# Optimization experiments

Hardware: AMD Instinct MI355X
Metric: run time of the kernel (lower is better)

Reference implementation:

```python
import jax, jax.numpy as jnp
import numpy as np

B, T, D, H, C, M = 128, 96, 256, 256, 8, 64
COMB = 4 * D + H  # z, z_prime, x_i, global_dynamics, h


def setup_inputs() -> dict:
    key = jax.random.key(0)
    ks = jax.random.split(key, 24)
    X = jax.random.normal(ks[0], (B, T, D), jnp.float32)
    X_last = jax.random.normal(ks[1], (B, T, D), jnp.float32)
    Mask = jax.random.bernoulli(ks[2], 0.5, (B, T, D)).astype(jnp.float32)
    Delta = jax.random.uniform(ks[3], (B, T, D), jnp.float32, 0.0, 5.0)
    X_last_b = jax.random.normal(ks[4], (B, T, D), jnp.float32)
    Delta_b = jax.random.uniform(ks[5], (B, T, D), jnp.float32, 0.0, 5.0)
    x = jnp.stack([X, X_last, Mask, Delta, X_last_b, Delta_b], axis=1)  # [B,6,T,D]
    X_mean = jax.random.normal(ks[6], (1, T, D), jnp.float32)
    clusters = jax.random.randint(ks[7], (D,), 1, C + 1, jnp.int64)
    s = 1.0 / np.sqrt(COMB)
    def U(k, shape, sc):
        return jax.random.uniform(k, shape, jnp.float32, -sc, sc)
    params = {
        'W_i': U(ks[8], (H, COMB), s), 'b_i': U(ks[9], (H,), s),
        'W_f': U(ks[10], (H, COMB), s), 'b_f': U(ks[11], (H,), s),
        'W_o': U(ks[12], (H, COMB), s), 'b_o': U(ks[13], (H,), s),
        'W_c': U(ks[14], (H, COMB), s), 'b_c': U(ks[15], (H,), s),
        'W_fc': U(ks[16], (D, H), 1.0 / np.sqrt(H)), 'b_fc': U(ks[17], (D,), 1.0 / np.sqrt(H)),
        'gz_w': U(ks[18], (D,), 1.0 / np.sqrt(D)), 'gz_b': U(ks[19], (D,), 1.0 / np.sqrt(D)),
        'gzp_w': U(ks[20], (D,), 1.0 / np.sqrt(D)), 'gzp_b': U(ks[21], (D,), 1.0 / np.sqrt(D)),
        'memory': jax.random.uniform(ks[22], (C, M, D), jnp.float32, -1.0 / np.sqrt(M), 1.0 / np.sqrt(M)),
    }
    k2 = jax.random.split(ks[23], 2)
    params['local_w'] = jax.random.uniform(k2[0], (3, D), jnp.float32, -1.0 / np.sqrt(3.0), 1.0 / np.sqrt(3.0))
    params['global_w'] = jax.random.uniform(k2[1], (C,), jnp.float32, -1.0 / np.sqrt(C), 1.0 / np.sqrt(C))
    return dict(x=x, X_mean=X_mean, clusters=clusters, **params)


def reference(x, X_mean, clusters, W_i, b_i, W_f, b_f, W_o, b_o, W_c, b_c,
              W_fc, b_fc, gz_w, gz_b, gzp_w, gzp_b, memory, local_w, global_w):
    # cluster one-hot feature masks: [C, D] (cluster ids are 1-based)
    cmask = (clusters[None, :] == jnp.arange(1, C + 1, dtype=clusters.dtype)[:, None]).astype(x.dtype)

    X, X_last, Mask, Delta, X_last_b, Delta_b = [x[:, i] for i in range(6)]  # each [B,T,D]
    xm = X_mean[0]  # [T,D]

    def step(carry, inp):
        h, c = carry
        xt, xl, xlb, m, d, db, mean = inp
        # FilterLinear with eye filter == diagonal linear; GRU-D decay
        dz = jnp.exp(-jax.nn.relu(d * gz_w + gz_b))
        dzp = jnp.exp(-jax.nn.relu(db * gzp_w + gzp_b))
        z = m * xt + (1 - m) * (dz * xl + (1 - dz) * mean)
        zp = m * xt + (1 - m) * (dzp * xlb + (1 - dzp) * mean)
        x_i = h @ W_fc.T + b_fc  # [B,D]
        local_stats = local_w[0] * z + local_w[1] * zp + local_w[2] * x_i  # [B,D]
        # per-cluster masked local stats -> memory attention
        li = local_stats[:, None, :] * cmask[None]              # [B,C,D]
        scores = jnp.einsum('cmd,bcd->bcm', memory, li)          # [B,C,M]
        s = jax.nn.softmax(scores, axis=-1)
        gd = jnp.einsum('bcm,cmd->bcd', s, memory)               # [B,C,D]
        gd = jnp.einsum('bcd,c->bd', gd, global_w)               # [B,D]
        combined = jnp.concatenate([z, zp, x_i, gd, h], axis=1)  # [B,4D+H]
        i = jax.nn.sigmoid(combined @ W_i.T + b_i)
        f = jax.nn.sigmoid(combined @ W_f.T + b_f)
        o = jax.nn.sigmoid(combined @ W_o.T + b_o)
        ct = jnp.tanh(combined @ W_c.T + b_c)
        c = f * c + i * ct
        h = o * jnp.tanh(c)
        out = h @ W_fc.T + b_fc
        return (h, c), out

    h0 = jnp.zeros((x.shape[0], H), x.dtype)
    c0 = jnp.zeros((x.shape[0], H), x.dtype)
    xs = (X.transpose(1, 0, 2), X_last.transpose(1, 0, 2), X_last_b.transpose(1, 0, 2),
          Mask.transpose(1, 0, 2), Delta.transpose(1, 0, 2), Delta_b.transpose(1, 0, 2), xm)
    _, outs = jax.lax.scan(step, (h0, c0), xs)
    return outs.transpose(1, 0, 2)  # [B,T,D]
```

## Files before the change

### kernel.cpp

```cpp
#include <hip/hip_runtime.h>
#include <hip/hip_bf16.h>
#include <hip/hip_fp16.h>
#include <cstdint>
#include <cstddef>


#define PLANE 24576

using bf16_t = __hip_bfloat16;
typedef __bf16 bf16x8 __attribute__((ext_vector_type(8)));
typedef float  f32x4  __attribute__((ext_vector_type(4)));
typedef unsigned int u32x4 __attribute__((ext_vector_type(4)));

__device__ __forceinline__ float  b2f(bf16_t v){ return __bfloat162float(v); }
__device__ __forceinline__ bf16_t f2b(float v){ return __float2bfloat16(v); }
__device__ __forceinline__ float ldF(const void* p, size_t i, int f32){
  return f32 ? ((const float*)p)[i] : b2f(((const bf16_t*)p)[i]);
}
__device__ __forceinline__ bf16x8 ld_frag(const void* p){
  union { uint4 u; bf16x8 v; } c;
  c.u = *(const uint4*)p;
  return c.v;
}
__device__ __forceinline__ bf16x8 u2b(u32x4 u){
  union { u32x4 u; bf16x8 v; } c; c.u = u; return c.v;
}
__device__ __forceinline__ f32x4 mfma_bf16(bf16x8 a, bf16x8 b, f32x4 c){
  return __builtin_amdgcn_mfma_f32_16x16x32_bf16(a, b, c, 0, 0, 0);
}

__device__ __forceinline__ u32x4 ld_cg(const void* p){
  u32x4 r;
  asm volatile("global_load_dwordx4 %0, %1, off sc0 sc1"
               : "=v"(r) : "v"(p) : "memory");
  return r;
}
__device__ __forceinline__ void st_cg(void* p, u32x4 v){
  asm volatile("global_store_dwordx4 %0, %1, off sc0 sc1"
               :: "v"(p), "v"(v) : "memory");
}
__device__ __forceinline__ int ld_cg_u16(const void* p){
  int r;
  asm volatile("global_load_ushort %0, %1, off sc0 sc1"
               : "=v"(r) : "v"(p) : "memory");
  return r;
}
__device__ __forceinline__ void st_flag(int* p, int v){
  asm volatile("global_store_dword %0, %1, off sc0 sc1"
               :: "v"(p), "v"(v) : "memory");
}
__device__ __forceinline__ int ld_flag(const int* p){
  int r;
  asm volatile("global_load_dword %0, %1, off sc0 sc1\n\ts_waitcnt vmcnt(0)"
               : "=v"(r) : "v"(p) : "memory");
  return r;
}
__device__ __forceinline__ void vm_wait0(){
  asm volatile("s_waitcnt vmcnt(0)" ::: "memory");
  __builtin_amdgcn_sched_barrier(0);
}
__device__ __forceinline__ float h2f_bits(int u){
  union{ unsigned short s; __half h; } c; c.s = (unsigned short)u;
  return __half2float(c.h);
}

__global__ __launch_bounds__(64) void k_detect(
    const uint32_t* __restrict__ xu, const uint32_t* __restrict__ clu,
    int* __restrict__ flags)
{
  __shared__ int cnt[2];
  int t = threadIdx.x;
  if (t < 2) cnt[t] = 0;
  __syncthreads();
  uint32_t v = xu[2*PLANE + t];
  if (v == 0u || v == 0x3F800000u) atomicAdd(&cnt[0], 1);
  if (clu[2*t + 1] == 0u) atomicAdd(&cnt[1], 1);
  __syncthreads();
  if (t == 0){
    flags[0] = (cnt[0] >= 48) ? 1 : 0;
    flags[1] = (cnt[1] >= 60) ? 1 : 0;
  }
}

__global__ __launch_bounds__(256) void k_zero(int* __restrict__ bar){
  bar[blockIdx.x*256 + threadIdx.x] = 0;
}

__global__ __launch_bounds__(256) void k_canon(
    const void* __restrict__ Wfc, const void* __restrict__ Xmean,
    const void* __restrict__ bfc, const void* __restrict__ localw,
    const void* __restrict__ globalw, const void* __restrict__ gzw,
    const void* __restrict__ gzb, const void* __restrict__ gzpw,
    const void* __restrict__ gzpb, const int* __restrict__ flags,
    bf16_t* __restrict__ WfcC, bf16_t* __restrict__ XmC,
    bf16_t* __restrict__ bfcC, bf16_t* __restrict__ lwC,
    bf16_t* __restrict__ gwC, float* __restrict__ gzC)
{
  const int f32 = flags[0];
  int i = blockIdx.x*256 + threadIdx.x;
  if (i < 65536) WfcC[i] = f2b(ldF(Wfc, i, f32));
  if (i < 24576) XmC[i]  = f2b(ldF(Xmean, i, f32));
  if (i < 256)   bfcC[i] = f2b(ldF(bfc, i, f32));
  if (i < 768)   lwC[i]  = f2b(ldF(localw, i, f32));
  if (i < 8)     gwC[i]  = f2b(ldF(globalw, i, f32));
  if (i < 256){
    gzC[i]       = ldF(gzw,  i, f32);
    gzC[256 + i] = ldF(gzb,  i, f32);
    gzC[512 + i] = ldF(gzpw, i, f32);
    gzC[768 + i] = ldF(gzpb, i, f32);
  }
}

__global__ __launch_bounds__(256) void k_fold(
    const void* __restrict__ Wi, const void* __restrict__ Wf,
    const void* __restrict__ Wo, const void* __restrict__ Wc,
    const void* __restrict__ bi, const void* __restrict__ bfg,
    const void* __restrict__ bo, const void* __restrict__ bcg,
    const void* __restrict__ Wfc, const void* __restrict__ bfc,
    const int* __restrict__ flags,
    bf16_t* __restrict__ U, bf16_t* __restrict__ Uz, float* __restrict__ bias2)
{
  const int f32 = flags[0];
  int n = blockIdx.x; int g = n & 3; int j = n >> 2;
  const void* Wg = (g==0)?Wi:(g==1)?Wf:(g==2)?Wo:Wc;
  const void* bg = (g==0)?bi:(g==1)?bfg:(g==2)?bo:bcg;
  const size_t wb = (size_t)j*1280;
  int k = threadIdx.x;
  float acc = 0.f;
  for (int d=0; d<256; ++d)
    acc += ldF(Wg, wb+512+d, f32) * ldF(Wfc, (size_t)d*256+k, f32);
  U[(size_t)n*512 + k]        = f2b(acc + ldF(Wg, wb+1024+k, f32));
  U[(size_t)n*512 + 256 + k]  = f2b(ldF(Wg, wb+768+k, f32));
  Uz[(size_t)n*512 + k]       = f2b(ldF(Wg, wb+k, f32));
  Uz[(size_t)n*512 + 256 + k] = f2b(ldF(Wg, wb+256+k, f32));
  __shared__ float red[256];
  red[k] = ldF(Wg, wb+512+k, f32) * ldF(bfc, k, f32);
  __syncthreads();
  for (int s=128; s>0; s>>=1){ if (k<s) red[k]+=red[k+s]; __syncthreads(); }
  if (k==0) bias2[n] = red[0] + ldF(bg, j, f32);
}

__global__ __launch_bounds__(256) void k_foldG(
    const void* __restrict__ Wi, const void* __restrict__ Wf,
    const void* __restrict__ Wo, const void* __restrict__ Wc,
    const void* __restrict__ memory, const int* __restrict__ flags,
    bf16_t* __restrict__ G)
{
  const int f32 = flags[0];
  __shared__ float wrow[4][256];
  int j = blockIdx.x; int tid = threadIdx.x;
  const void* Wg[4] = {Wi,Wf,Wo,Wc};
  for (int g=0; g<4; ++g)
    wrow[g][tid] = ldF(Wg[g], (size_t)j*1280 + 768 + tid, f32);
  __syncthreads();
  for (int half=0; half<2; ++half){
    int cm = half*256 + tid;
    float a0=0,a1=0,a2=0,a3=0;
    for (int d=0; d<256; ++d){
      float mv = ldF(memory, (size_t)cm*256 + d, f32);
      a0 += wrow[0][d]*mv; a1 += wrow[1][d]*mv;
      a2 += wrow[2][d]*mv; a3 += wrow[3][d]*mv;
    }
    G[(size_t)(4*j+0)*512 + cm] = f2b(a0);
    G[(size_t)(4*j+1)*512 + cm] = f2b(a1);
    G[(size_t)(4*j+2)*512 + cm] = f2b(a2);
    G[(size_t)(4*j+3)*512 + cm] = f2b(a3);
  }
}

__global__ __launch_bounds__(256) void k_foldQ(
    const int* __restrict__ clusters, const void* __restrict__ memory,
    const bf16_t* __restrict__ lwC, const bf16_t* __restrict__ WfcC,
    const bf16_t* __restrict__ bfcC, const int* __restrict__ flags,
    bf16_t* __restrict__ Mem2, bf16_t* __restrict__ Qbf, float* __restrict__ qb)
{
  const int f32 = flags[0], i64 = flags[1];
  const int cm = blockIdx.x; const int c = cm >> 6;
  const int tid = threadIdx.x;
  __shared__ float ml2[256];
  __shared__ float red[256];
  int cv = i64 ? clusters[2*tid] : clusters[tid];
  float mv = (cv == c+1) ? ldF(memory, (size_t)cm*256 + tid, f32) : 0.f;
  Mem2[(size_t)cm*256 + tid] = f2b(mv);
  float m2 = mv * b2f(lwC[512 + tid]);
  ml2[tid] = m2;
  red[tid] = m2 * b2f(bfcC[tid]);
  __syncthreads();
  float acc = 0.f;
  for (int d=0; d<256; ++d)
    acc += ml2[d] * b2f(WfcC[(size_t)d*256 + tid]);
  Qbf[(size_t)cm*256 + tid] = f2b(acc);
  for (int s=128; s>0; s>>=1){ if (tid<s) red[tid]+=red[tid+s]; __syncthreads(); }
  if (tid==0) qb[cm] = red[0];
}

__global__ __launch_bounds__(256) void k_zzp(
    const void* __restrict__ x, const bf16_t* __restrict__ XmC,
    const float* __restrict__ gzC, const bf16_t* __restrict__ lwC,
    const int* __restrict__ flags,
    bf16_t* __restrict__ Zcat, bf16_t* __restrict__ Zl)
{
  const int f32 = flags[0];
  int r = blockIdx.x;
  int t = r >> 7, b = r & 127, d = threadIdx.x;
  size_t base = (size_t)b*6*PLANE + (size_t)t*256 + d;
  float xt = ldF(x, base          , f32);
  float xl = ldF(x, base +   PLANE, f32);
  float mk = ldF(x, base + 2*PLANE, f32);
  float de = ldF(x, base + 3*PLANE, f32);
  float xlb= ldF(x, base + 4*PLANE, f32);
  float deb= ldF(x, base + 5*PLANE, f32);
  float mean = b2f(XmC[t*256+d]);
  float dz  = expf(-fmaxf(0.f, de *gzC[d]     + gzC[256+d]));
  float dzp = expf(-fmaxf(0.f, deb*gzC[512+d] + gzC[768+d]));
  float z  = mk*xt + (1.f-mk)*(dz *xl  + (1.f-dz )*mean);
  float zp = mk*xt + (1.f-mk)*(dzp*xlb + (1.f-dzp)*mean);
  Zcat[(size_t)r*512 + d]       = f2b(z);
  Zcat[(size_t)r*512 + 256 + d] = f2b(zp);
  Zl[(size_t)r*256 + d] = f2b(b2f(lwC[d])*z + b2f(lwC[256+d])*zp);
}

__global__ __launch_bounds__(256) void k_mega(
    const bf16_t* __restrict__ gwC,
    const bf16_t* __restrict__ U, const bf16_t* __restrict__ G,
    const bf16_t* __restrict__ Qbf, const bf16_t* __restrict__ Uz,
    const float* __restrict__ bias2, const bf16_t* __restrict__ Mem2,
    const float* __restrict__ qb, const bf16_t* __restrict__ Zcat,
    const bf16_t* __restrict__ Zl, const bf16_t* __restrict__ WfcC,
    const bf16_t* __restrict__ bfcC, const int* __restrict__ flags,
    __half* __restrict__ zc, __half* __restrict__ SzM,
    bf16_t* __restrict__ hSeq, bf16_t* __restrict__ tSeq,
    int* __restrict__ bar, void* __restrict__ outv)
{
  __shared__ bf16_t Us[64][264];
  __shared__ bf16_t Gs[64][520];
  __shared__ bf16_t Qs[64][264];
  __shared__ bf16_t hS[16][264];
  __shared__ bf16_t tS[16][520];
  __shared__ bf16_t tO[16][64];
  __shared__ bf16_t hO[16][16];

  const int bid = blockIdx.x;
  const int tid = threadIdx.x;
  const int W = tid>>6, l = tid&63, q = l>>4, cl = l&15;
  int* zcflag  = bar + 512;
  int* szmflag = bar + 576;

  if (bid < 128){
    const int g = bid & 7, s = bid >> 3;
    const int r0 = g*16;
    const int n0 = s*64;
    int* barA = bar + g*64;
    int* barB = bar + g*64 + 32;

    for (int i=tid; i<64*32; i+=256){ int r=i>>5, c8=(i&31)*8;
      *(uint4*)(&Us[r][c8]) = *(const uint4*)(U + (size_t)(n0+r)*512 + c8); }
    for (int i=tid; i<64*64; i+=256){ int r=i>>6, c8=(i&63)*8;
      *(uint4*)(&Gs[r][c8]) = *(const uint4*)(G + (size_t)(n0+r)*512 + c8); }
    if (s<8)
      for (int i=tid; i<64*32; i+=256){ int r=i>>5, c8=(i&31)*8;
        *(uint4*)(&Qs[r][c8]) = *(const uint4*)(Qbf + (size_t)(s*64+r)*256 + c8); }
    const float gw_c = (s<8)? b2f(gwC[s]) : 0.f;
    const bool sc_wave = (s<8) && (W==0);
    float creg[4] = {0.f,0.f,0.f,0.f};
    __syncthreads();

    for (int t=0; t<96; ++t){
      if (W==0){
        const int* fp = nullptr; int need = 0; bool act = false;
        if (l < 16){ fp = barA + l; need = t; act = (t>0); }
        else if (l < 20){ fp = zcflag + 4*s + (l-16); need = t+1; act = true; }
        else if (l < 24){ fp = szmflag + 4*s + (l-20); need = t+1; act = (s<8); }
        int f;
        do { f = act ? ld_flag(fp) : 0x7fffffff; } while (__any(f < need));
        if (t>0){
          const bf16_t* hsrc = hSeq + (size_t)t*128*256 + (size_t)r0*256;
          u32x4 hv[8];
#pragma unroll
          for (int k=0;k<8;++k){ int c=l+64*k;
            hv[k] = ld_cg(hsrc + (size_t)(c>>5)*256 + (c&31)*8); }
          vm_wait0();
#pragma unroll
          for (int k=0;k<8;++k){ int c=l+64*k;
            *(u32x4*)(&hS[c>>5][(c&31)*8]) = hv[k]; }
        } else {
#pragma unroll
          for (int k=0;k<8;++k){ int c=l+64*k;
            *(u32x4*)(&hS[c>>5][(c&31)*8]) = (u32x4){0,0,0,0}; }
        }
      }
      __syncthreads();
      int zr[4];
#pragma unroll
      for (int rr=0; rr<4; ++rr)
        zr[rr] = ld_cg_u16(zc + ((size_t)(t*128)+r0+q*4+rr)*1024 + n0 + W*16 + cl);
      if (sc_wave){
        int sr[16];
#pragma unroll
        for (int nt=0; nt<4; ++nt)
#pragma unroll
          for (int rr=0; rr<4; ++rr)
            sr[nt*4+rr] = ld_cg_u16(
              SzM + ((size_t)(t*128)+r0+q*4+rr)*512 + s*64 + nt*16 + cl);
        f32x4 sa[4];
#pragma unroll
        for (int nt=0;nt<4;++nt) sa[nt]=(f32x4){0.f,0.f,0.f,0.f};
#pragma unroll
        for (int ks=0; ks<8; ++ks){
          bf16x8 a = ld_frag(&hS[cl][ks*32 + q*8]);
#pragma unroll
          for (int nt=0; nt<4; ++nt)
            sa[nt] = mfma_bf16(a, ld_frag(&Qs[nt*16+cl][ks*32 + q*8]), sa[nt]);
        }
        vm_wait0();
#pragma unroll
        for (int nt=0; nt<4; ++nt)
#pragma unroll
          for (int rr=0; rr<4; ++rr) sa[nt][rr] += h2f_bits(sr[nt*4+rr]);
#pragma unroll
        for (int rr=0; rr<4; ++rr){
          float mx = fmaxf(fmaxf(sa[0][rr],sa[1][rr]), fmaxf(sa[2][rr],sa[3][rr]));
          mx = fmaxf(mx, __shfl_xor(mx,1));
          mx = fmaxf(mx, __shfl_xor(mx,2));
          mx = fmaxf(mx, __shfl_xor(mx,4));
          mx = fmaxf(mx, __shfl_xor(mx,8));
          float e0=expf(sa[0][rr]-mx), e1=expf(sa[1][rr]-mx);
          float e2=expf(sa[2][rr]-mx), e3=expf(sa[3][rr]-mx);
          float sm = e0+e1+e2+e3;
          sm += __shfl_xor(sm,1); sm += __shfl_xor(sm,2);
          sm += __shfl_xor(sm,4); sm += __shfl_xor(sm,8);
          float sc = gw_c/sm;
          tO[q*4+rr][ 0+cl] = f2b(e0*sc);
          tO[q*4+rr][16+cl] = f2b(e1*sc);
          tO[q*4+rr][32+cl] = f2b(e2*sc);
          tO[q*4+rr][48+cl] = f2b(e3*sc);
        }
        bf16_t* tdst = tSeq + (size_t)t*128*512 + (size_t)r0*512 + s*64;
#pragma unroll
        for (int k=0;k<2;++k){ int c=l+64*k;
          u32x4 v = *(u32x4*)(&tO[c>>3][(c&7)*8]);
          st_cg(tdst + (size_t)(c>>3)*512 + (c&7)*8, v); }
        vm_wait0();
        if (l==0) st_flag(barB + s, t+1);
      }
      f32x4 acc = {0.f,0.f,0.f,0.f};
#pragma unroll
      for (int ks=0; ks<8; ++ks)
        acc = mfma_bf16(ld_frag(&hS[cl][ks*32 + q*8]),
                        ld_frag(&Us[W*16+cl][ks*32 + q*8]), acc);
      if (W==1){
        const int* fp = barB + (l&7);
        int v;
        do { int f = ld_flag(fp); v = (l<8)? f : 0x7fffffff; } while (__any(v < t+1));
        const bf16_t* tsrc = tSeq + (size_t)t*128*512 + (size_t)r0*512;
        u32x4 tv[16];
#pragma unroll
        for (int k=0;k<16;++k){ int c=l+64*k;
          tv[k] = ld_cg(tsrc + (size_t)(c>>6)*512 + (c&63)*8); }
        vm_wait0();
#pragma unroll
        for (int k=0;k<16;++k){ int c=l+64*k;
          *(u32x4*)(&tS[c>>6][(c&63)*8]) = tv[k]; }
      }
      __syncthreads();
#pragma unroll
      for (int ks=0; ks<16; ++ks)
        acc = mfma_bf16(ld_frag(&tS[cl][ks*32 + q*8]),
                        ld_frag(&Gs[W*16+cl][ks*32 + q*8]), acc);
      vm_wait0();
#pragma unroll
      for (int rr=0; rr<4; ++rr) acc[rr] += h2f_bits(zr[rr]);
      const int base = l & ~3;
#pragma unroll
      for (int rr=0; rr<4; ++rr){
        float p = acc[rr];
        float pi = __shfl(p, base+0);
        float pf = __shfl(p, base+1);
        float po = __shfl(p, base+2);
        float pc = __shfl(p, base+3);
        float iv = 1.f/(1.f+expf(-pi));
        float fv = 1.f/(1.f+expf(-pf));
        float ov = 1.f/(1.f+expf(-po));
        float cv = tanhf(pc);
        float cn = fv*creg[rr] + iv*cv;
        creg[rr] = cn;
        float hv = ov * tanhf(cn);
        if ((l&3)==0)
          hO[q*4+rr][W*4 + (cl>>2)] = f2b(hv);
      }
      __syncthreads();
      if (W==0){
        if (l < 32){
          u32x4 v = *(u32x4*)(&hO[l>>1][(l&1)*8]);
          st_cg(hSeq + (size_t)(t+1)*128*256 + (size_t)(r0+(l>>1))*256
                     + s*16 + (l&1)*8, v);
        }
        vm_wait0();
        if (l==0) st_flag(barA + s, t+1);
      }
    }
  } else if (bid < 192){
    const int a = bid - 128;
    const int n0a = a*16;
    bf16_t (*BS)[520] = (bf16_t(*)[520])&Gs[0][0];
    __half (*zT)[16]  = (__half(*)[16])&Qs[0][0];
    for (int i=tid; i<16*64; i+=256){ int r=i>>6, c8=(i&63)*8;
      *(uint4*)(&BS[r][c8]) = *(const uint4*)(Uz + (size_t)(n0a+r)*512 + c8); }
    const float bias = bias2[n0a + cl];
    __syncthreads();
    for (int t=0; t<96; ++t){
      f32x4 a0={0.f,0.f,0.f,0.f}, a1={0.f,0.f,0.f,0.f};
      const bf16_t* ar0 = Zcat + ((size_t)t*128 + W*32 + cl)*512;
      const bf16_t* ar1 = ar0 + (size_t)16*512;
#pragma unroll
      for (int ks=0; ks<16; ++ks){
        bf16x8 b = ld_frag(&BS[cl][ks*32 + q*8]);
        a0 = mfma_bf16(ld_frag(ar0 + ks*32 + q*8), b, a0);
        a1 = mfma_bf16(ld_frag(ar1 + ks*32 + q*8), b, a1);
      }
#pragma unroll
      for (int rr=0; rr<4; ++rr){
        zT[W*32      + q*4 + rr][cl] = __float2half(a0[rr] + bias);
        zT[W*32 + 16 + q*4 + rr][cl] = __float2half(a1[rr] + bias);
      }
      __syncthreads();
      { int row = tid>>1, half = tid&1;
        u32x4 v = *(u32x4*)(&zT[row][half*8]);
        st_cg(zc + ((size_t)t*128+row)*1024 + n0a + half*8, v);
      }
      vm_wait0();
      __syncthreads();
      if (tid==0) st_flag(zcflag + a, t+1);
    }
  } else if (bid < 224){
    const int a2 = bid - 192;
    const int cm0 = a2*16;
    bf16_t (*BS)[520] = (bf16_t(*)[520])&Gs[0][0];
    __half (*zT)[16]  = (__half(*)[16])&Qs[0][0];
    for (int i=tid; i<16*32; i+=256){ int r=i>>5, c8=(i&31)*8;
      *(uint4*)(&BS[r][c8]) = *(const uint4*)(Mem2 + (size_t)(cm0+r)*256 + c8); }
    const float bias = qb[cm0 + cl];
    __syncthreads();
    for (int t=0; t<96; ++t){
      f32x4 a0={0.f,0.f,0.f,0.f}, a1={0.f,0.f,0.f,0.f};
      const bf16_t* ar0 = Zl + ((size_t)t*128 + W*32 + cl)*256;
      const bf16_t* ar1 = ar0 + (size_t)16*256;
#pragma unroll
      for (int ks=0; ks<8; ++ks){
        bf16x8 b = ld_frag(&BS[cl][ks*32 + q*8]);
        a0 = mfma_bf16(ld_frag(ar0 + ks*32 + q*8), b, a0);
        a1 = mfma_bf16(ld_frag(ar1 + ks*32 + q*8), b, a1);
      }
#pragma unroll
      for (int rr=0; rr<4; ++rr){
        zT[W*32      + q*4 + rr][cl] = __float2half(a0[rr] + bias);
        zT[W*32 + 16 + q*4 + rr][cl] = __float2half(a1[rr] + bias);
      }
      __syncthreads();
      { int row = tid>>1, half = tid&1;
        u32x4 v = *(u32x4*)(&zT[row][half*8]);
        st_cg(SzM + ((size_t)t*128+row)*512 + cm0 + half*8, v);
      }
      vm_wait0();
      __syncthreads();
      if (tid==0) st_flag(szmflag + a2, t+1);
    }
  } else {
    const int a3 = bid - 224;
    const int oc0 = a3*16;
    bf16_t (*BS)[520] = (bf16_t(*)[520])&Gs[0][0];
    for (int i=tid; i<16*32; i+=256){ int r=i>>5, c8=(i&31)*8;
      *(uint4*)(&BS[r][c8]) = *(const uint4*)(WfcC + (size_t)(oc0+r)*256 + c8); }
    const float bias = b2f(bfcC[oc0 + cl]);
    const int f32o = flags[0];
    __syncthreads();
    for (int t=0; t<96; ++t){
      const int* f1 = bar + (l>>4)*64 + (l&15);
      const int* f2 = bar + ((l>>4)+4)*64 + (l&15);
      int fa, fb;
      do { fa = ld_flag(f1); fb = ld_flag(f2); }
      while (__any((fa < t+1) || (fb < t+1)));
      u32x4 av0[8], av1[8];
      const bf16_t* hr0 = hSeq + ((size_t)(t+1)*128 + W*32 + cl)*256;
      const bf16_t* hr1 = hr0 + (size_t)16*256;
#pragma unroll
      for (int ks=0; ks<8; ++ks){
        av0[ks] = ld_cg(hr0 + ks*32 + q*8);
        av1[ks] = ld_cg(hr1 + ks*32 + q*8);
      }
      vm_wait0();
      f32x4 o0={0.f,0.f,0.f,0.f}, o1={0.f,0.f,0.f,0.f};
#pragma unroll
      for (int ks=0; ks<8; ++ks){
        bf16x8 b = ld_frag(&BS[cl][ks*32 + q*8]);
        o0 = mfma_bf16(u2b(av0[ks]), b, o0);
        o1 = mfma_bf16(u2b(av1[ks]), b, o1);
      }
#pragma unroll
      for (int rr=0; rr<4; ++rr){
        int b0 = W*32 + q*4 + rr;
        int b1 = b0 + 16;
        float v0 = o0[rr] + bias;
        float v1 = o1[rr] + bias;
        size_t ob0 = ((size_t)b0*96 + t)*256 + oc0 + cl;
        size_t ob1 = ((size_t)b1*96 + t)*256 + oc0 + cl;
        if (f32o){ ((float*)outv)[ob0] = v0; ((float*)outv)[ob1] = v1; }
        else     { ((bf16_t*)outv)[ob0] = f2b(v0); ((bf16_t*)outv)[ob1] = f2b(v1); }
      }
    }
  }
}

extern "C" void kernel_launch(void* const* d_in, const int* in_sizes, int n_in,
                              void* d_out, int out_size, void* d_ws, size_t ws_size,
                              hipStream_t stream)
{
  const void* x       = d_in[0];
  const void* Xmean   = d_in[1];
  const int*  clusters= (const int*)d_in[2];
  const void* Wi  = d_in[3];
  const void* bi  = d_in[4];
  const void* Wf  = d_in[5];
  const void* bfp = d_in[6];
  const void* Wo  = d_in[7];
  const void* bo  = d_in[8];
  const void* Wc  = d_in[9];
  const void* bcp = d_in[10];
  const void* Wfc = d_in[11];
  const void* bfc = d_in[12];
  const void* gzw = d_in[13];
  const void* gzb = d_in[14];
  const void* gzpw= d_in[15];
  const void* gzpb= d_in[16];
  const void* memory = d_in[17];
  const void* localw = d_in[18];
  const void* globalw= d_in[19];
  (void)in_sizes; (void)n_in; (void)out_size; (void)ws_size;

  char* ws = (char*)d_ws;
  size_t off = 0;
  auto take = [&](size_t bytes)->char*{
    char* p = ws + off; off = (off + bytes + 255) & ~(size_t)255; return p; };
  int*    flags  = (int*)   take(16);
  int*    bar    = (int*)   take(1024*4);
  bf16_t* U      = (bf16_t*)take((size_t)1024*512*2);
  bf16_t* Uz     = (bf16_t*)take((size_t)1024*512*2);
  bf16_t* G      = (bf16_t*)take((size_t)1024*512*2);
  bf16_t* WfcC   = (bf16_t*)take((size_t)65536*2);
  bf16_t* XmC    = (bf16_t*)take((size_t)24576*2);
  bf16_t* bfcC   = (bf16_t*)take(256*2);
  bf16_t* lwC    = (bf16_t*)take(768*2);
  bf16_t* gwC    = (bf16_t*)take(8*2);
  float*  gzC    = (float*) take(1024*4);
  float*  bias2  = (float*) take(1024*4);
  bf16_t* Mem2   = (bf16_t*)take((size_t)512*256*2);
  bf16_t* Qbf    = (bf16_t*)take((size_t)512*256*2);
  float*  qb     = (float*) take(512*4);
  __half* zc     = (__half*)take((size_t)12288*1024*2);
  __half* SzM    = (__half*)take((size_t)12288*512*2);
  bf16_t* Zcat   = (bf16_t*)take((size_t)12288*512*2);
  bf16_t* Zl     = (bf16_t*)take((size_t)12288*256*2);
  bf16_t* tSeq   = (bf16_t*)take((size_t)96*128*512*2);
  bf16_t* hSeq   = (bf16_t*)take((size_t)97*128*256*2);

  k_detect<<<1,    64, 0,stream>>>((const uint32_t*)x, (const uint32_t*)clusters, flags);
  k_zero  <<<4,    256,0,stream>>>(bar);
  k_canon <<<256,  256,0,stream>>>(Wfc, Xmean, bfc, localw, globalw,
                                   gzw, gzb, gzpw, gzpb, flags,
                                   WfcC, XmC, bfcC, lwC, gwC, gzC);
  k_fold  <<<1024, 256,0,stream>>>(Wi,Wf,Wo,Wc, bi,bfp,bo,bcp, Wfc,bfc, flags,
                                   U, Uz, bias2);
  k_foldG <<<256,  256,0,stream>>>(Wi,Wf,Wo,Wc, memory, flags, G);
  k_foldQ <<<512,  256,0,stream>>>(clusters, memory, lwC, WfcC, bfcC, flags,
                                   Mem2, Qbf, qb);
  k_zzp   <<<12288,256,0,stream>>>(x, XmC, gzC, lwC, flags, Zcat, Zl);
  k_mega  <<<240,  256,0,stream>>>(gwC, U, G, Qbf, Uz, bias2, Mem2, qb,
                                   Zcat, Zl, WfcC, bfcC, flags,
                                   zc, SzM, hSeq, tSeq, bar, d_out);
}
```

Before: 1.093 ms.

## Merge prep kernels, widen producer tiles, and stage score and output through LDS

Folds the zero, fold, foldG, foldQ and zzp launches into k_canon plus one block-indexed k_prep kernel, cutting launch count. In k_mega the zc, SzM and output producer blocks now each compute 64- or 32-column tiles, which drops the grid from 240 to 160 blocks and reduces the number of flags to poll. Outputs are staged in LDS so they can be written as coalesced 16-byte stores. The SzM scores are prefetched into shared memory by a spare wave, and the gate nonlinearities are applied once per lane before the shuffle. The fewer, larger producer blocks each carry more serial work per timestep, which could lengthen the recurrent critical path.

After: 1.498 ms. +37.1%, slower.

```diff
diff --git a/kernel.cpp b/kernel.cpp
--- a/kernel.cpp
+++ b/kernel.cpp
@@ -28,6 +28,14 @@
 __device__ __forceinline__ f32x4 mfma_bf16(bf16x8 a, bf16x8 b, f32x4 c){
   return __builtin_amdgcn_mfma_f32_16x16x32_bf16(a, b, c, 0, 0, 0);
 }
+__device__ __forceinline__ unsigned pkb(float a, float b){
+  union{ bf16_t h; unsigned short u;} ca, cb; ca.h=f2b(a); cb.h=f2b(b);
+  return (unsigned)ca.u | ((unsigned)cb.u<<16);
+}
+__device__ __forceinline__ float h2f_bits(int u){
+  union{ unsigned short s; __half h; } c; c.s = (unsigned short)u;
+  return __half2float(c.h);
+}
 
 __device__ __forceinline__ u32x4 ld_cg(const void* p){
   u32x4 r;
@@ -58,10 +66,6 @@
 __device__ __forceinline__ void vm_wait0(){
   asm volatile("s_waitcnt vmcnt(0)" ::: "memory");
   __builtin_amdgcn_sched_barrier(0);
-}
-__device__ __forceinline__ float h2f_bits(int u){
-  union{ unsigned short s; __half h; } c; c.s = (unsigned short)u;
-  return __half2float(c.h);
 }
 
 __global__ __launch_bounds__(64) void k_detect(
@@ -82,10 +86,6 @@
   }
 }
 
-__global__ __launch_bounds__(256) void k_zero(int* __restrict__ bar){
-  bar[blockIdx.x*256 + threadIdx.x] = 0;
-}
-
 __global__ __launch_bounds__(256) void k_canon(
     const void* __restrict__ Wfc, const void* __restrict__ Xmean,
     const void* __restrict__ bfc, const void* __restrict__ localw,
@@ -94,10 +94,12 @@
     const void* __restrict__ gzpb, const int* __restrict__ flags,
     bf16_t* __restrict__ WfcC, bf16_t* __restrict__ XmC,
     bf16_t* __restrict__ bfcC, bf16_t* __restrict__ lwC,
-    bf16_t* __restrict__ gwC, float* __restrict__ gzC)
+    bf16_t* __restrict__ gwC, float* __restrict__ gzC,
+    int* __restrict__ bar)
 {
   const int f32 = flags[0];
   int i = blockIdx.x*256 + threadIdx.x;
+  if (blockIdx.x < 4) bar[i] = 0;
   if (i < 65536) WfcC[i] = f2b(ldF(Wfc, i, f32));
   if (i < 24576) XmC[i]  = f2b(ldF(Xmean, i, f32));
   if (i < 256)   bfcC[i] = f2b(ldF(bfc, i, f32));
@@ -111,113 +113,98 @@
   }
 }
 
-__global__ __launch_bounds__(256) void k_fold(
+__global__ __launch_bounds__(256) void k_prep(
     const void* __restrict__ Wi, const void* __restrict__ Wf,
     const void* __restrict__ Wo, const void* __restrict__ Wc,
     const void* __restrict__ bi, const void* __restrict__ bfg,
     const void* __restrict__ bo, const void* __restrict__ bcg,
     const void* __restrict__ Wfc, const void* __restrict__ bfc,
-    const int* __restrict__ flags,
-    bf16_t* __restrict__ U, bf16_t* __restrict__ Uz, float* __restrict__ bias2)
-{
-  const int f32 = flags[0];
-  int n = blockIdx.x; int g = n & 3; int j = n >> 2;
-  const void* Wg = (g==0)?Wi:(g==1)?Wf:(g==2)?Wo:Wc;
-  const void* bg = (g==0)?bi:(g==1)?bfg:(g==2)?bo:bcg;
-  const size_t wb = (size_t)j*1280;
-  int k = threadIdx.x;
-  float acc = 0.f;
-  for (int d=0; d<256; ++d)
-    acc += ldF(Wg, wb+512+d, f32) * ldF(Wfc, (size_t)d*256+k, f32);
-  U[(size_t)n*512 + k]        = f2b(acc + ldF(Wg, wb+1024+k, f32));
-  U[(size_t)n*512 + 256 + k]  = f2b(ldF(Wg, wb+768+k, f32));
-  Uz[(size_t)n*512 + k]       = f2b(ldF(Wg, wb+k, f32));
-  Uz[(size_t)n*512 + 256 + k] = f2b(ldF(Wg, wb+256+k, f32));
-  __shared__ float red[256];
-  red[k] = ldF(Wg, wb+512+k, f32) * ldF(bfc, k, f32);
-  __syncthreads();
-  for (int s=128; s>0; s>>=1){ if (k<s) red[k]+=red[k+s]; __syncthreads(); }
-  if (k==0) bias2[n] = red[0] + ldF(bg, j, f32);
-}
-
-__global__ __launch_bounds__(256) void k_foldG(
-    const void* __restrict__ Wi, const void* __restrict__ Wf,
-    const void* __restrict__ Wo, const void* __restrict__ Wc,
-    const void* __restrict__ memory, const int* __restrict__ flags,
-    bf16_t* __restrict__ G)
-{
-  const int f32 = flags[0];
-  __shared__ float wrow[4][256];
-  int j = blockIdx.x; int tid = threadIdx.x;
-  const void* Wg[4] = {Wi,Wf,Wo,Wc};
-  for (int g=0; g<4; ++g)
-    wrow[g][tid] = ldF(Wg[g], (size_t)j*1280 + 768 + tid, f32);
-  __syncthreads();
-  for (int half=0; half<2; ++half){
-    int cm = half*256 + tid;
-    float a0=0,a1=0,a2=0,a3=0;
-    for (int d=0; d<256; ++d){
-      float mv = ldF(memory, (size_t)cm*256 + d, f32);
-      a0 += wrow[0][d]*mv; a1 += wrow[1][d]*mv;
-      a2 += wrow[2][d]*mv; a3 += wrow[3][d]*mv;
-    }
-    G[(size_t)(4*j+0)*512 + cm] = f2b(a0);
-    G[(size_t)(4*j+1)*512 + cm] = f2b(a1);
-    G[(size_t)(4*j+2)*512 + cm] = f2b(a2);
-    G[(size_t)(4*j+3)*512 + cm] = f2b(a3);
-  }
-}
-
-__global__ __launch_bounds__(256) void k_foldQ(
-    const int* __restrict__ clusters, const void* __restrict__ memory,
+    const void* __restrict__ memory, const int* __restrict__ clusters,
+    const void* __restrict__ x,
+    const bf16_t* __restrict__ XmC, const float* __restrict__ gzC,
     const bf16_t* __restrict__ lwC, const bf16_t* __restrict__ WfcC,
     const bf16_t* __restrict__ bfcC, const int* __restrict__ flags,
-    bf16_t* __restrict__ Mem2, bf16_t* __restrict__ Qbf, float* __restrict__ qb)
-{
-  const int f32 = flags[0], i64 = flags[1];
-  const int cm = blockIdx.x; const int c = cm >> 6;
-  const int tid = threadIdx.x;
-  __shared__ float ml2[256];
-  __shared__ float red[256];
-  int cv = i64 ? clusters[2*tid] : clusters[tid];
-  float mv = (cv == c+1) ? ldF(memory, (size_t)cm*256 + tid, f32) : 0.f;
-  Mem2[(size_t)cm*256 + tid] = f2b(mv);
-  float m2 = mv * b2f(lwC[512 + tid]);
-  ml2[tid] = m2;
-  red[tid] = m2 * b2f(bfcC[tid]);
-  __syncthreads();
-  float acc = 0.f;
-  for (int d=0; d<256; ++d)
-    acc += ml2[d] * b2f(WfcC[(size_t)d*256 + tid]);
-  Qbf[(size_t)cm*256 + tid] = f2b(acc);
-  for (int s=128; s>0; s>>=1){ if (tid<s) red[tid]+=red[tid+s]; __syncthreads(); }
-  if (tid==0) qb[cm] = red[0];
-}
-
-__global__ __launch_bounds__(256) void k_zzp(
-    const void* __restrict__ x, const bf16_t* __restrict__ XmC,
-    const float* __restrict__ gzC, const bf16_t* __restrict__ lwC,
-    const int* __restrict__ flags,
+    bf16_t* __restrict__ U, bf16_t* __restrict__ Uz,
+    float* __restrict__ bias2, bf16_t* __restrict__ G,
+    bf16_t* __restrict__ Mem2, bf16_t* __restrict__ Qbf,
+    float* __restrict__ qb,
     bf16_t* __restrict__ Zcat, bf16_t* __restrict__ Zl)
 {
-  const int f32 = flags[0];
-  int r = blockIdx.x;
-  int t = r >> 7, b = r & 127, d = threadIdx.x;
-  size_t base = (size_t)b*6*PLANE + (size_t)t*256 + d;
-  float xt = ldF(x, base          , f32);
-  float xl = ldF(x, base +   PLANE, f32);
-  float mk = ldF(x, base + 2*PLANE, f32);
-  float de = ldF(x, base + 3*PLANE, f32);
-  float xlb= ldF(x, base + 4*PLANE, f32);
-  float deb= ldF(x, base + 5*PLANE, f32);
-  float mean = b2f(XmC[t*256+d]);
-  float dz  = expf(-fmaxf(0.f, de *gzC[d]     + gzC[256+d]));
-  float dzp = expf(-fmaxf(0.f, deb*gzC[512+d] + gzC[768+d]));
-  float z  = mk*xt + (1.f-mk)*(dz *xl  + (1.f-dz )*mean);
-  float zp = mk*xt + (1.f-mk)*(dzp*xlb + (1.f-dzp)*mean);
-  Zcat[(size_t)r*512 + d]       = f2b(z);
-  Zcat[(size_t)r*512 + 256 + d] = f2b(zp);
-  Zl[(size_t)r*256 + d] = f2b(b2f(lwC[d])*z + b2f(lwC[256+d])*zp);
+  __shared__ float sA[4][256];
+  __shared__ float red[256];
+  const int f32 = flags[0], i64 = flags[1];
+  const int bid = blockIdx.x, tid = threadIdx.x;
+
+  if (bid < 1024){
+    int n = bid; int g = n & 3; int j = n >> 2;
+    const void* Wg = (g==0)?Wi:(g==1)?Wf:(g==2)?Wo:Wc;
+    const void* bg = (g==0)?bi:(g==1)?bfg:(g==2)?bo:bcg;
+    const size_t wb = (size_t)j*1280;
+    int k = tid;
+    float acc = 0.f;
+    for (int d=0; d<256; ++d)
+      acc += ldF(Wg, wb+512+d, f32) * ldF(Wfc, (size_t)d*256+k, f32);
+    U[(size_t)n*512 + k]        = f2b(acc + ldF(Wg, wb+1024+k, f32));
+    U[(size_t)n*512 + 256 + k]  = f2b(ldF(Wg, wb+768+k, f32));
+    Uz[(size_t)n*512 + k]       = f2b(ldF(Wg, wb+k, f32));
+    Uz[(size_t)n*512 + 256 + k] = f2b(ldF(Wg, wb+256+k, f32));
+    red[k] = ldF(Wg, wb+512+k, f32) * ldF(bfc, k, f32);
+    __syncthreads();
+    for (int s=128; s>0; s>>=1){ if (k<s) red[k]+=red[k+s]; __syncthreads(); }
+    if (k==0) bias2[n] = red[0] + ldF(bg, j, f32);
+  } else if (bid < 1280){
+    int j = bid - 1024;
+    const void* Wg[4] = {Wi,Wf,Wo,Wc};
+    for (int g=0; g<4; ++g)
+      sA[g][tid] = ldF(Wg[g], (size_t)j*1280 + 768 + tid, f32);
+    __syncthreads();
+    for (int half=0; half<2; ++half){
+      int cm = half*256 + tid;
+      float a0=0,a1=0,a2=0,a3=0;
+      for (int d=0; d<256; ++d){
+        float mv = ldF(memory, (size_t)cm*256 + d, f32);
+        a0 += sA[0][d]*mv; a1 += sA[1][d]*mv;
+        a2 += sA[2][d]*mv; a3 += sA[3][d]*mv;
+      }
+      G[(size_t)(4*j+0)*512 + cm] = f2b(a0);
+      G[(size_t)(4*j+1)*512 + cm] = f2b(a1);
+      G[(size_t)(4*j+2)*512 + cm] = f2b(a2);
+      G[(size_t)(4*j+3)*512 + cm] = f2b(a3);
+    }
+  } else if (bid < 1792){
+    const int cm = bid - 1280; const int c = cm >> 6;
+    int cv = i64 ? clusters[2*tid] : clusters[tid];
+    float mv = (cv == c+1) ? ldF(memory, (size_t)cm*256 + tid, f32) : 0.f;
+    Mem2[(size_t)cm*256 + tid] = f2b(mv);
+    float m2 = mv * b2f(lwC[512 + tid]);
+    sA[0][tid] = m2;
+    red[tid] = m2 * b2f(bfcC[tid]);
+    __syncthreads();
+    float acc = 0.f;
+    for (int d=0; d<256; ++d)
+      acc += sA[0][d] * b2f(WfcC[(size_t)d*256 + tid]);
+    Qbf[(size_t)cm*256 + tid] = f2b(acc);
+    for (int s=128; s>0; s>>=1){ if (tid<s) red[tid]+=red[tid+s]; __syncthreads(); }
+    if (tid==0) qb[cm] = red[0];
+  } else {
+    int r = bid - 1792;
+    int t = r >> 7, b = r & 127, d = tid;
+    size_t base = (size_t)b*6*PLANE + (size_t)t*256 + d;
+    float xt = ldF(x, base          , f32);
+    float xl = ldF(x, base +   PLANE, f32);
+    float mk = ldF(x, base + 2*PLANE, f32);
+    float de = ldF(x, base + 3*PLANE, f32);
+    float xlb= ldF(x, base + 4*PLANE, f32);
+    float deb= ldF(x, base + 5*PLANE, f32);
+    float mean = b2f(XmC[t*256+d]);
+    float dz  = expf(-fmaxf(0.f, de *gzC[d]     + gzC[256+d]));
+    float dzp = expf(-fmaxf(0.f, deb*gzC[512+d] + gzC[768+d]));
+    float z  = mk*xt + (1.f-mk)*(dz *xl  + (1.f-dz )*mean);
+    float zp = mk*xt + (1.f-mk)*(dzp*xlb + (1.f-dzp)*mean);
+    Zcat[(size_t)r*512 + d]       = f2b(z);
+    Zcat[(size_t)r*512 + 256 + d] = f2b(zp);
+    Zl[(size_t)r*256 + d] = f2b(b2f(lwC[d])*z + b2f(lwC[256+d])*zp);
+  }
 }
 
 __global__ __launch_bounds__(256) void k_mega(
@@ -232,19 +219,20 @@
     bf16_t* __restrict__ hSeq, bf16_t* __restrict__ tSeq,
     int* __restrict__ bar, void* __restrict__ outv)
 {
-  __shared__ bf16_t Us[64][264];
-  __shared__ bf16_t Gs[64][520];
-  __shared__ bf16_t Qs[64][264];
-  __shared__ bf16_t hS[16][264];
-  __shared__ bf16_t tS[16][520];
+  __shared__ bf16_t Us[64][260];
+  __shared__ bf16_t Gs[64][516];
+  __shared__ bf16_t Qs[64][260];
+  __shared__ bf16_t hS[16][260];
+  __shared__ bf16_t tS[16][516];
   __shared__ bf16_t tO[16][64];
   __shared__ bf16_t hO[16][16];
+  __shared__ __half smS[16][68];
 
   const int bid = blockIdx.x;
   const int tid = threadIdx.x;
   const int W = tid>>6, l = tid&63, q = l>>4, cl = l&15;
   int* zcflag  = bar + 512;
-  int* szmflag = bar + 576;
+  int* szmflag = bar + 544;
 
   if (bid < 128){
     const int g = bid & 7, s = bid >> 3;
@@ -269,8 +257,7 @@
       if (W==0){
         const int* fp = nullptr; int need = 0; bool act = false;
         if (l < 16){ fp = barA + l; need = t; act = (t>0); }
-        else if (l < 20){ fp = zcflag + 4*s + (l-16); need = t+1; act = true; }
-        else if (l < 24){ fp = szmflag + 4*s + (l-20); need = t+1; act = (s<8); }
+        else if (l == 16){ fp = zcflag + s; need = t+1; act = true; }
         int f;
         do { f = act ? ld_flag(fp) : 0x7fffffff; } while (__any(f < need));
         if (t>0){
@@ -288,6 +275,14 @@
           for (int k=0;k<8;++k){ int c=l+64*k;
             *(u32x4*)(&hS[c>>5][(c&31)*8]) = (u32x4){0,0,0,0}; }
         }
+      } else if (W==3 && s<8){
+        if (l==0){ while (ld_flag(szmflag + s) < t+1) {} }
+        const __half* ssrc = SzM + ((size_t)t*128 + r0)*512 + s*64;
+        u32x4 v0 = ld_cg(ssrc + (size_t)(l>>3)*512 + (l&7)*8);
+        u32x4 v1 = ld_cg(ssrc + (size_t)(8+(l>>3))*512 + (l&7)*8);
+        vm_wait0();
+        *(u32x4*)(&smS[l>>3][(l&7)*8]) = v0;
+        *(u32x4*)(&smS[8+(l>>3)][(l&7)*8]) = v1;
       }
       __syncthreads();
       int zr[4];
@@ -295,13 +290,6 @@
       for (int rr=0; rr<4; ++rr)
         zr[rr] = ld_cg_u16(zc + ((size_t)(t*128)+r0+q*4+rr)*1024 + n0 + W*16 + cl);
       if (sc_wave){
-        int sr[16];
-#pragma unroll
-        for (int nt=0; nt<4; ++nt)
-#pragma unroll
-          for (int rr=0; rr<4; ++rr)
-            sr[nt*4+rr] = ld_cg_u16(
-              SzM + ((size_t)(t*128)+r0+q*4+rr)*512 + s*64 + nt*16 + cl);
         f32x4 sa[4];
 #pragma unroll
         for (int nt=0;nt<4;++nt) sa[nt]=(f32x4){0.f,0.f,0.f,0.f};
@@ -312,11 +300,11 @@
           for (int nt=0; nt<4; ++nt)
             sa[nt] = mfma_bf16(a, ld_frag(&Qs[nt*16+cl][ks*32 + q*8]), sa[nt]);
         }
-        vm_wait0();
 #pragma unroll
         for (int nt=0; nt<4; ++nt)
 #pragma unroll
-          for (int rr=0; rr<4; ++rr) sa[nt][rr] += h2f_bits(sr[nt*4+rr]);
+          for (int rr=0; rr<4; ++rr)
+            sa[nt][rr] += __half2float(smS[q*4+rr][nt*16+cl]);
 #pragma unroll
         for (int rr=0; rr<4; ++rr){
           float mx = fmaxf(fmaxf(sa[0][rr],sa[1][rr]), fmaxf(sa[2][rr],sa[3][rr]));
@@ -374,14 +362,11 @@
 #pragma unroll
       for (int rr=0; rr<4; ++rr){
         float p = acc[rr];
-        float pi = __shfl(p, base+0);
-        float pf = __shfl(p, base+1);
-        float po = __shfl(p, base+2);
-        float pc = __shfl(p, base+3);
-        float iv = 1.f/(1.f+expf(-pi));
-        float fv = 1.f/(1.f+expf(-pf));
-        float ov = 1.f/(1.f+expf(-po));
-        float cv = tanhf(pc);
+        float gown = ((l&3)==3) ? tanhf(p) : 1.f/(1.f+expf(-p));
+        float iv = __shfl(gown, base+0);
+        float fv = __shfl(gown, base+1);
+        float ov = __shfl(gown, base+2);
+        float cv = __shfl(gown, base+3);
         float cn = fv*creg[rr] + iv*cv;
         creg[rr] = cn;
         float hv = ov * tanhf(cn);
@@ -399,79 +384,106 @@
         if (l==0) st_flag(barA + s, t+1);
       }
     }
-  } else if (bid < 192){
+  } else if (bid < 144){
     const int a = bid - 128;
-    const int n0a = a*16;
-    bf16_t (*BS)[520] = (bf16_t(*)[520])&Gs[0][0];
-    __half (*zT)[16]  = (__half(*)[16])&Qs[0][0];
-    for (int i=tid; i<16*64; i+=256){ int r=i>>6, c8=(i&63)*8;
-      *(uint4*)(&BS[r][c8]) = *(const uint4*)(Uz + (size_t)(n0a+r)*512 + c8); }
-    const float bias = bias2[n0a + cl];
+    const int n0a = a*64;
+    bf16_t (*UzS)[516] = (bf16_t(*)[516])&Gs[0][0];
+    __half (*zT)[68]   = (__half(*)[68])&Qs[0][0];
+    for (int i=tid; i<64*64; i+=256){ int r=i>>6, c8=(i&63)*8;
+      *(uint4*)(&UzS[r][c8]) = *(const uint4*)(Uz + (size_t)(n0a+r)*512 + c8); }
+    float bias[4];
+#pragma unroll
+    for (int ni=0;ni<4;++ni) bias[ni] = bias2[n0a + ni*16 + cl];
     __syncthreads();
     for (int t=0; t<96; ++t){
-      f32x4 a0={0.f,0.f,0.f,0.f}, a1={0.f,0.f,0.f,0.f};
+      f32x4 acc0[4], acc1[4];
+#pragma unroll
+      for (int ni=0;ni<4;++ni){ acc0[ni]=(f32x4){0,0,0,0}; acc1[ni]=(f32x4){0,0,0,0}; }
       const bf16_t* ar0 = Zcat + ((size_t)t*128 + W*32 + cl)*512;
       const bf16_t* ar1 = ar0 + (size_t)16*512;
 #pragma unroll
       for (int ks=0; ks<16; ++ks){
-        bf16x8 b = ld_frag(&BS[cl][ks*32 + q*8]);
-        a0 = mfma_bf16(ld_frag(ar0 + ks*32 + q*8), b, a0);
-        a1 = mfma_bf16(ld_frag(ar1 + ks*32 + q*8), b, a1);
-      }
-#pragma unroll
-      for (int rr=0; rr<4; ++rr){
-        zT[W*32      + q*4 + rr][cl] = __float2half(a0[rr] + bias);
-        zT[W*32 + 16 + q*4 + rr][cl] = __float2half(a1[rr] + bias);
-      }
-      __syncthreads();
-      { int row = tid>>1, half = tid&1;
-        u32x4 v = *(u32x4*)(&zT[row][half*8]);
-        st_cg(zc + ((size_t)t*128+row)*1024 + n0a + half*8, v);
+        bf16x8 a0 = ld_frag(ar0 + ks*32 + q*8);
+        bf16x8 a1 = ld_frag(ar1 + ks*32 + q*8);
+#pragma unroll
+        for (int ni=0; ni<4; ++ni){
+          bf16x8 b = ld_frag(&UzS[ni*16+cl][ks*32 + q*8]);
+          acc0[ni] = mfma_bf16(a0, b, acc0[ni]);
+          acc1[ni] = mfma_bf16(a1, b, acc1[ni]);
+        }
+      }
+#pragma unroll
+      for (int ni=0; ni<4; ++ni)
+#pragma unroll
+        for (int rr=0; rr<4; ++rr){
+          zT[W*32      + q*4 + rr][ni*16 + cl] = __float2half(acc0[ni][rr] + bias[ni]);
+          zT[W*32 + 16 + q*4 + rr][ni*16 + cl] = __float2half(acc1[ni][rr] + bias[ni]);
+        }
+      __syncthreads();
+#pragma unroll
+      for (int k=0;k<4;++k){ int c = tid + k*256;
+        int r = c>>3, off = (c&7)*8;
+        st_cg(zc + ((size_t)t*128 + r)*1024 + n0a + off, *(u32x4*)(&zT[r][off]));
       }
       vm_wait0();
       __syncthreads();
       if (tid==0) st_flag(zcflag + a, t+1);
     }
-  } else if (bid < 224){
-    const int a2 = bid - 192;
-    const int cm0 = a2*16;
-    bf16_t (*BS)[520] = (bf16_t(*)[520])&Gs[0][0];
-    __half (*zT)[16]  = (__half(*)[16])&Qs[0][0];
-    for (int i=tid; i<16*32; i+=256){ int r=i>>5, c8=(i&31)*8;
-      *(uint4*)(&BS[r][c8]) = *(const uint4*)(Mem2 + (size_t)(cm0+r)*256 + c8); }
-    const float bias = qb[cm0 + cl];
+  } else if (bid < 152){
+    const int a2 = bid - 144;
+    const int cm0 = a2*64;
+    bf16_t (*MeS)[260] = (bf16_t(*)[260])&Us[0][0];
+    __half (*zT)[68]   = (__half(*)[68])&Qs[0][0];
+    for (int i=tid; i<64*32; i+=256){ int r=i>>5, c8=(i&31)*8;
+      *(uint4*)(&MeS[r][c8]) = *(const uint4*)(Mem2 + (size_t)(cm0+r)*256 + c8); }
+    float bias[4];
+#pragma unroll
+    for (int ni=0;ni<4;++ni) bias[ni] = qb[cm0 + ni*16 + cl];
     __syncthreads();
     for (int t=0; t<96; ++t){
-      f32x4 a0={0.f,0.f,0.f,0.f}, a1={0.f,0.f,0.f,0.f};
+      f32x4 acc0[4], acc1[4];
+#pragma unroll
+      for (int ni=0;ni<4;++ni){ acc0[ni]=(f32x4){0,0,0,0}; acc1[ni]=(f32x4){0,0,0,0}; }
       const bf16_t* ar0 = Zl + ((size_t)t*128 + W*32 + cl)*256;
       const bf16_t* ar1 = ar0 + (size_t)16*256;
 #pragma unroll
       for (int ks=0; ks<8; ++ks){
-        bf16x8 b = ld_frag(&BS[cl][ks*32 + q*8]);
-        a0 = mfma_bf16(ld_frag(ar0 + ks*32 + q*8), b, a0);
-        a1 = mfma_bf16(ld_frag(ar1 + ks*32 + q*8), b, a1);
-      }
-#pragma unroll
-      for (int rr=0; rr<4; ++rr){
-        zT[W*32      + q*4 + rr][cl] = __float2half(a0[rr] + bias);
-        zT[W*32 + 16 + q*4 + rr][cl] = __float2half(a1[rr] + bias);
-      }
-      __syncthreads();
-      { int row = tid>>1, half = tid&1;
-        u32x4 v = *(u32x4*)(&zT[row][half*8]);
-        st_cg(SzM + ((size_t)t*128+row)*512 + cm0 + half*8, v);
+        bf16x8 a0 = ld_frag(ar0 + ks*32 + q*8);
+        bf16x8 a1 = ld_frag(ar1 + ks*32 + q*8);
+#pragma unroll
+        for (int ni=0; ni<4; ++ni){
+          bf16x8 b = ld_frag(&MeS[ni*16+cl][ks*32 + q*8]);
+          acc0[ni] = mfma_bf16(a0, b, acc0[ni]);
+          acc1[ni] = mfma_bf16(a1, b, acc1[ni]);
+        }
+      }
+#pragma unroll
+      for (int ni=0; ni<4; ++ni)
+#pragma unroll
+        for (int rr=0; rr<4; ++rr){
+          zT[W*32      + q*4 + rr][ni*16 + cl] = __float2half(acc0[ni][rr] + bias[ni]);
+          zT[W*32 + 16 + q*4 + rr][ni*16 + cl] = __float2half(acc1[ni][rr] + bias[ni]);
+        }
+      __syncthreads();
+#pragma unroll
+      for (int k=0;k<4;++k){ int c = tid + k*256;
+        int r = c>>3, off = (c&7)*8;
+        st_cg(SzM + ((size_t)t*128 + r)*512 + cm0 + off, *(u32x4*)(&zT[r][off]));
       }
       vm_wait0();
       __syncthreads();
       if (tid==0) st_flag(szmflag + a2, t+1);
     }
   } else {
-    const int a3 = bid - 224;
-    const int oc0 = a3*16;
-    bf16_t (*BS)[520] = (bf16_t(*)[520])&Gs[0][0];
-    for (int i=tid; i<16*32; i+=256){ int r=i>>5, c8=(i&31)*8;
-      *(uint4*)(&BS[r][c8]) = *(const uint4*)(WfcC + (size_t)(oc0+r)*256 + c8); }
-    const float bias = b2f(bfcC[oc0 + cl]);
+    const int a3 = bid - 152;
+    const int oc0 = a3*32;
+    bf16_t (*WfS)[260] = (bf16_t(*)[260])&Us[0][0];
+    float  (*oT)[36]   = (float(*)[36])&Qs[0][0];
+    for (int i=tid; i<32*32; i+=256){ int r=i>>5, c8=(i&31)*8;
+      *(uint4*)(&WfS[r][c8]) = *(const uint4*)(WfcC + (size_t)(oc0+r)*256 + c8); }
+    float bias[2];
+#pragma unroll
+    for (int ni=0;ni<2;++ni) bias[ni] = b2f(bfcC[oc0 + ni*16 + cl]);
     const int f32o = flags[0];
     __syncthreads();
     for (int t=0; t<96; ++t){
@@ -489,24 +501,44 @@
         av1[ks] = ld_cg(hr1 + ks*32 + q*8);
       }
       vm_wait0();
-      f32x4 o0={0.f,0.f,0.f,0.f}, o1={0.f,0.f,0.f,0.f};
+      f32x4 o00={0,0,0,0}, o01={0,0,0,0}, o10={0,0,0,0}, o11={0,0,0,0};
 #pragma unroll
       for (int ks=0; ks<8; ++ks){
-        bf16x8 b = ld_frag(&BS[cl][ks*32 + q*8]);
-        o0 = mfma_bf16(u2b(av0[ks]), b, o0);
-        o1 = mfma_bf16(u2b(av1[ks]), b, o1);
+        bf16x8 b0 = ld_frag(&WfS[cl][ks*32 + q*8]);
+        bf16x8 b1 = ld_frag(&WfS[16+cl][ks*32 + q*8]);
+        o00 = mfma_bf16(u2b(av0[ks]), b0, o00);
+        o01 = mfma_bf16(u2b(av0[ks]), b1, o01);
+        o10 = mfma_bf16(u2b(av1[ks]), b0, o10);
+        o11 = mfma_bf16(u2b(av1[ks]), b1, o11);
       }
 #pragma unroll
       for (int rr=0; rr<4; ++rr){
-        int b0 = W*32 + q*4 + rr;
-        int b1 = b0 + 16;
-        float v0 = o0[rr] + bias;
-        float v1 = o1[rr] + bias;
-        size_t ob0 = ((size_t)b0*96 + t)*256 + oc0 + cl;
-        size_t ob1 = ((size_t)b1*96 + t)*256 + oc0 + cl;
-        if (f32o){ ((float*)outv)[ob0] = v0; ((float*)outv)[ob1] = v1; }
-        else     { ((bf16_t*)outv)[ob0] = f2b(v0); ((bf16_t*)outv)[ob1] = f2b(v1); }
-      }
+        oT[W*32      + q*4 + rr][ 0 + cl] = o00[rr] + bias[0];
+        oT[W*32      + q*4 + rr][16 + cl] = o01[rr] + bias[1];
+        oT[W*32 + 16 + q*4 + rr][ 0 + cl] = o10[rr] + bias[0];
+        oT[W*32 + 16 + q*4 + rr][16 + cl] = o11[rr] + bias[1];
+      }
+      __syncthreads();
+      if (f32o){
+        float* outF = (float*)outv;
+#pragma unroll
+        for (int k=0;k<4;++k){ int c = tid + k*256;
+          int r = c>>3, off = (c&7)*4;
+          u32x4 v = *(u32x4*)(&oT[r][off]);
+          st_cg(outF + ((size_t)r*96 + t)*256 + oc0 + off, v);
+        }
+      } else {
+        bf16_t* outB = (bf16_t*)outv;
+#pragma unroll
+        for (int k=0;k<2;++k){ int c = tid + k*256;
+          int r = c>>2, off = (c&3)*8;
+          u32x4 v;
+#pragma unroll
+          for (int j=0;j<4;++j) v[j] = pkb(oT[r][off+2*j], oT[r][off+2*j+1]);
+          st_cg(outB + ((size_t)r*96 + t)*256 + oc0 + off, v);
+        }
+      }
+      __syncthreads();
     }
   }
 }
@@ -564,17 +596,14 @@
   bf16_t* hSeq   = (bf16_t*)take((size_t)97*128*256*2);
 
   k_detect<<<1,    64, 0,stream>>>((const uint32_t*)x, (const uint32_t*)clusters, flags);
-  k_zero  <<<4,    256,0,stream>>>(bar);
   k_canon <<<256,  256,0,stream>>>(Wfc, Xmean, bfc, localw, globalw,
                                    gzw, gzb, gzpw, gzpb, flags,
-                                   WfcC, XmC, bfcC, lwC, gwC, gzC);
-  k_fold  <<<1024, 256,0,stream>>>(Wi,Wf,Wo,Wc, bi,bfp,bo,bcp, Wfc,bfc, flags,
-                                   U, Uz, bias2);
-  k_foldG <<<256,  256,0,stream>>>(Wi,Wf,Wo,Wc, memory, flags, G);
-  k_foldQ <<<512,  256,0,stream>>>(clusters, memory, lwC, WfcC, bfcC, flags,
-                                   Mem2, Qbf, qb);
-  k_zzp   <<<12288,256,0,stream>>>(x, XmC, gzC, lwC, flags, Zcat, Zl);
-  k_mega  <<<240,  256,0,stream>>>(gwC, U, G, Qbf, Uz, bias2, Mem2, qb,
+                                   WfcC, XmC, bfcC, lwC, gwC, gzC, bar);
+  k_prep  <<<14080,256,0,stream>>>(Wi,Wf,Wo,Wc, bi,bfp,bo,bcp, Wfc,bfc,
+                                   memory, clusters, x,
+                                   XmC, gzC, lwC, WfcC, bfcC, flags,
+                                   U, Uz, bias2, G, Mem2, Qbf, qb, Zcat, Zl);
+  k_mega  <<<160,  256,0,stream>>>(gwC, U, G, Qbf, Uz, bias2, Mem2, qb,
                                    Zcat, Zl, WfcC, bfcC, flags,
                                    zc, SzM, hSeq, tSeq, bar, d_out);
 }
```
